# Performance work log

Measured on AMD Instinct MI355X. Metric: run time of the kernel, lower is better.

Reference implementation:

```python
import jax, jax.numpy as jnp
import numpy as np
import math

EPS = 1.1920929e-07  # torch F.rms_norm default eps = fp32 machine epsilon


def rms_norm(x):
    # normalize over last dim, no learned weight (matches F.rms_norm(x, (d,)))
    var = jnp.mean(jnp.square(x), axis=-1, keepdims=True)
    return x * jax.lax.rsqrt(var + EPS)


def rotary(x, cos, sin):
    # x: (B, T, H, D); cos/sin: (T, D) -> broadcast over B, H
    d2 = x.shape[-1] // 2
    x1, x2 = x[..., :d2], x[..., d2:]
    rot = jnp.concatenate([-x2, x1], axis=-1)  # rotate_half
    c = cos[None, :, None, :]
    s = sin[None, :, None, :]
    return x * c + rot * s


def setup_inputs() -> dict:
    key = jax.random.key(0)
    ks = jax.random.split(key, 5)
    B, T, C, H = 2, 2048, 1024, 16
    D = C // H
    x = jax.random.normal(ks[0], (B, T, C), dtype=jnp.float32)
    # real RoPE tables (theta=10000), duplicated across the two halves
    inv_freq = 1.0 / (10000.0 ** (np.arange(0, D, 2, dtype=np.float32) / D))
    pos = np.arange(T, dtype=np.float32)
    freqs = np.outer(pos, inv_freq)            # (T, D/2)
    emb = np.concatenate([freqs, freqs], -1)   # (T, D)
    cos = jnp.asarray(np.cos(emb), dtype=jnp.float32)
    sin = jnp.asarray(np.sin(emb), dtype=jnp.float32)
    sc_in = 1.0 / math.sqrt(C)
    W_attn = jax.random.normal(ks[1], (C, 3 * C), dtype=jnp.float32) * sc_in
    b_attn = jax.random.normal(ks[2], (3 * C,), dtype=jnp.float32) * 0.02
    W_proj = jax.random.normal(ks[3], (C, C), dtype=jnp.float32) * sc_in
    b_proj = jax.random.normal(ks[4], (C,), dtype=jnp.float32) * 0.02
    return {"x": x, "cos": cos, "sin": sin, "W_attn": W_attn, "b_attn": b_attn,
            "W_proj": W_proj, "b_proj": b_proj}


def reference(x, cos, sin, W_attn, b_attn, W_proj, b_proj):
    B, T, C = x.shape
    H = 16
    D = C // H
    qkv = x @ W_attn + b_attn                         # (B, T, 3C)
    qkv = qkv.reshape(B, T, 3, H, D)                  # 'b t (a h d) -> ...'
    q, k, v = qkv[:, :, 0], qkv[:, :, 1], qkv[:, :, 2]  # (B, T, H, D)
    q, k = rms_norm(q), rms_norm(k)
    q = rotary(q, cos, sin)
    k = rotary(k, cos, sin)
    # causal SDPA, scale = 1/sqrt(D)
    scale = 1.0 / math.sqrt(D)
    scores = jnp.einsum('bthd,bshd->bhts', q, k) * scale  # (B, H, T, T)
    causal = jnp.tril(jnp.ones((T, T), dtype=bool))
    scores = jnp.where(causal[None, None], scores, jnp.finfo(scores.dtype).min)
    attn = jax.nn.softmax(scores, axis=-1)
    y = jnp.einsum('bhts,bshd->bthd', attn, v)            # (B, T, H, D)
    y = y.reshape(B, T, C)
    return y @ W_proj + b_proj
```

## Files before the change

### kernel.cpp

```cpp
#include <hip/hip_runtime.h>
#include <math.h>

#define EPSV 1.1920929e-07f

typedef __attribute__((ext_vector_type(8))) short short8;
typedef __attribute__((ext_vector_type(4))) float f32x4;

__device__ __forceinline__ float bf2f(unsigned short u) {
    union { unsigned int i; float f; } c; c.i = ((unsigned int)u) << 16; return c.f;
}
__device__ __forceinline__ unsigned short f2bf(float f) {
    union { float f; unsigned int i; } c; c.f = f;
    unsigned int r = c.i + 0x7FFFu + ((c.i >> 16) & 1u);
    return (unsigned short)(r >> 16);
}
__device__ __forceinline__ unsigned int pack_bf16_ru(float a, float b) {
    union { float f; unsigned int i; } ca, cb; ca.f = a; cb.f = b;
    return __builtin_amdgcn_perm(cb.i + 0x8000u, ca.i + 0x8000u, 0x07060302u);
}
__device__ __forceinline__ void async_lds16(const unsigned short* g, unsigned short* l) {
    __builtin_amdgcn_global_load_lds(
        (const __attribute__((address_space(1))) unsigned int*)g,
        (__attribute__((address_space(3))) unsigned int*)l, 16, 0, 0);
}

__global__ __launch_bounds__(256) void cast_bf16(
    const float* __restrict__ src, unsigned short* __restrict__ dst, int n)
{
    const int i = (blockIdx.x * 256 + threadIdx.x) * 4;
    if (i >= n) return;
    const float4 v = *(const float4*)&src[i];
    ushort4 o;
    o.x = f2bf(v.x); o.y = f2bf(v.y); o.z = f2bf(v.z); o.w = f2bf(v.w);
    *(ushort4*)&dst[i] = o;
}

__global__ __launch_bounds__(256) void transpose_cast_both(
    const float* __restrict__ Wa, unsigned short* __restrict__ Wat,
    const float* __restrict__ Wp, unsigned short* __restrict__ Wpt)
{
    __shared__ float tile[32][33];
    int bx = blockIdx.x;
    const float* W; unsigned short* Wt; int N;
    if (bx < 96) { W = Wa; Wt = Wat; N = 3072; }
    else         { W = Wp; Wt = Wpt; N = 1024; bx -= 96; }
    const int n0 = bx * 32, k0 = blockIdx.y * 32;
    const int r = threadIdx.x >> 3, c4 = (threadIdx.x & 7) * 4;
    const float4 v = *(const float4*)&W[(size_t)(k0 + r) * N + n0 + c4];
    tile[r][c4 + 0] = v.x; tile[r][c4 + 1] = v.y;
    tile[r][c4 + 2] = v.z; tile[r][c4 + 3] = v.w;
    __syncthreads();
    ushort4 o;
    o.x = f2bf(tile[c4 + 0][r]); o.y = f2bf(tile[c4 + 1][r]);
    o.z = f2bf(tile[c4 + 2][r]); o.w = f2bf(tile[c4 + 3][r]);
    *(ushort4*)&Wt[(size_t)(n0 + r) * 1024 + k0 + c4] = o;
}

template <bool OUT_BF16>
__global__ __launch_bounds__(256) void gemm_bf16(
    const unsigned short* __restrict__ A,
    const unsigned short* __restrict__ Bt,
    const float* __restrict__ bias,
    void* __restrict__ Cv,
    int M, int N, int K)
{
    __shared__ unsigned short As0[128][32], As1[128][32];
    __shared__ unsigned short Bs0[128][32], Bs1[128][32];
    const int t    = threadIdx.x;
    const int lane = t & 63;
    const int wv   = t >> 6;
    const int wrow = (wv >> 1) * 64;
    const int wcol = (wv & 1) * 64;
    const int m0 = blockIdx.y * 128;
    const int n0 = blockIdx.x * 128;
    const int col  = lane & 15;
    const int quad = lane >> 4;

    const int srow = (wv << 5) + (lane >> 2);
    const int scol = (lane & 3) << 3;
    const unsigned short* a00 = A  + (size_t)(m0 + srow) * K + scol;
    const unsigned short* a10 = a00 + (size_t)16 * K;
    const unsigned short* a01 = a00 + 32;
    const unsigned short* a11 = a10 + 32;
    const unsigned short* b00 = Bt + (size_t)(n0 + srow) * K + scol;
    const unsigned short* b10 = b00 + (size_t)16 * K;
    const unsigned short* b01 = b00 + 32;
    const unsigned short* b11 = b10 + 32;
    unsigned short* al0 = &As0[srow][scol];
    unsigned short* al1 = &As0[srow + 16][scol];
    unsigned short* al2 = &As1[srow][scol];
    unsigned short* al3 = &As1[srow + 16][scol];
    unsigned short* bl0 = &Bs0[srow][scol];
    unsigned short* bl1 = &Bs0[srow + 16][scol];
    unsigned short* bl2 = &Bs1[srow][scol];
    unsigned short* bl3 = &Bs1[srow + 16][scol];

    f32x4 acc[4][4];
    #pragma unroll
    for (int i = 0; i < 4; ++i)
        #pragma unroll
        for (int j = 0; j < 4; ++j)
            acc[i][j] = (f32x4){0.f, 0.f, 0.f, 0.f};

    for (int k0 = 0; k0 < K; k0 += 64) {
        async_lds16(a00, al0);
        async_lds16(a10, al1);
        async_lds16(a01, al2);
        async_lds16(a11, al3);
        async_lds16(b00, bl0);
        async_lds16(b10, bl1);
        async_lds16(b01, bl2);
        async_lds16(b11, bl3);
        a00 += 64; a10 += 64; a01 += 64; a11 += 64;
        b00 += 64; b10 += 64; b01 += 64; b11 += 64;
        __syncthreads();
        short8 af[2][4], bf[2][4];
        #pragma unroll
        for (int mt = 0; mt < 4; ++mt) {
            af[0][mt] = *(const short8*)&As0[wrow + mt * 16 + col][quad << 3];
            af[1][mt] = *(const short8*)&As1[wrow + mt * 16 + col][quad << 3];
        }
        #pragma unroll
        for (int nt = 0; nt < 4; ++nt) {
            bf[0][nt] = *(const short8*)&Bs0[wcol + nt * 16 + col][quad << 3];
            bf[1][nt] = *(const short8*)&Bs1[wcol + nt * 16 + col][quad << 3];
        }
        #pragma unroll
        for (int ks = 0; ks < 2; ++ks)
            #pragma unroll
            for (int mt = 0; mt < 4; ++mt)
                #pragma unroll
                for (int nt = 0; nt < 4; ++nt)
                    acc[mt][nt] = __builtin_amdgcn_mfma_f32_16x16x32_bf16(
                        af[ks][mt], bf[ks][nt], acc[mt][nt], 0, 0, 0);
        __syncthreads();
    }

    const int rowq = quad << 2;
    #pragma unroll
    for (int nt = 0; nt < 4; ++nt) {
        const int n = n0 + wcol + nt * 16 + col;
        const float bv = bias[n];
        #pragma unroll
        for (int mt = 0; mt < 4; ++mt) {
            #pragma unroll
            for (int r = 0; r < 4; ++r) {
                const int m = m0 + wrow + mt * 16 + rowq + r;
                const float v = acc[mt][nt][r] + bv;
                if (OUT_BF16)
                    ((unsigned short*)Cv)[(size_t)m * N + n] = f2bf(v);
                else
                    ((float*)Cv)[(size_t)m * N + n] = v;
            }
        }
    }
}

__global__ __launch_bounds__(256) void gemm_bf16_n64(
    const unsigned short* __restrict__ A,
    const unsigned short* __restrict__ Bt,
    const float* __restrict__ bias,
    float* __restrict__ C,
    int M, int N, int K)
{
    __shared__ unsigned short As0[128][32], As1[128][32];
    __shared__ unsigned short Bs0[64][32], Bs1[64][32];
    const int t    = threadIdx.x;
    const int lane = t & 63;
    const int wv   = t >> 6;
    const int wrow = wv << 5;
    const int m0 = blockIdx.y * 128;
    const int n0 = blockIdx.x * 64;
    const int col  = lane & 15;
    const int quad = lane >> 4;

    const int srow = (wv << 5) + (lane >> 2);
    const int scol = (lane & 3) << 3;
    const unsigned short* a00 = A  + (size_t)(m0 + srow) * K + scol;
    const unsigned short* a10 = a00 + (size_t)16 * K;
    const unsigned short* a01 = a00 + 32;
    const unsigned short* a11 = a10 + 32;
    const int bsrow = (wv << 4) + (lane >> 2);
    const unsigned short* b00 = Bt + (size_t)(n0 + bsrow) * K + scol;
    const unsigned short* b01 = b00 + 32;
    unsigned short* al0 = &As0[srow][scol];
    unsigned short* al1 = &As0[srow + 16][scol];
    unsigned short* al2 = &As1[srow][scol];
    unsigned short* al3 = &As1[srow + 16][scol];
    unsigned short* bl0 = &Bs0[bsrow][scol];
    unsigned short* bl1 = &Bs1[bsrow][scol];

    f32x4 acc[2][4];
    #pragma unroll
    for (int i = 0; i < 2; ++i)
        #pragma unroll
        for (int j = 0; j < 4; ++j)
            acc[i][j] = (f32x4){0.f, 0.f, 0.f, 0.f};

    for (int k0 = 0; k0 < K; k0 += 64) {
        async_lds16(a00, al0);
        async_lds16(a10, al1);
        async_lds16(a01, al2);
        async_lds16(a11, al3);
        async_lds16(b00, bl0);
        async_lds16(b01, bl1);
        a00 += 64; a10 += 64; a01 += 64; a11 += 64;
        b00 += 64; b01 += 64;
        __syncthreads();
        short8 af[2][2], bf[2][4];
        #pragma unroll
        for (int mt = 0; mt < 2; ++mt) {
            af[0][mt] = *(const short8*)&As0[wrow + mt * 16 + col][quad << 3];
            af[1][mt] = *(const short8*)&As1[wrow + mt * 16 + col][quad << 3];
        }
        #pragma unroll
        for (int nt = 0; nt < 4; ++nt) {
            bf[0][nt] = *(const short8*)&Bs0[nt * 16 + col][quad << 3];
            bf[1][nt] = *(const short8*)&Bs1[nt * 16 + col][quad << 3];
        }
        #pragma unroll
        for (int ks = 0; ks < 2; ++ks)
            #pragma unroll
            for (int mt = 0; mt < 2; ++mt)
                #pragma unroll
                for (int nt = 0; nt < 4; ++nt)
                    acc[mt][nt] = __builtin_amdgcn_mfma_f32_16x16x32_bf16(
                        af[ks][mt], bf[ks][nt], acc[mt][nt], 0, 0, 0);
        __syncthreads();
    }

    const int rowq = quad << 2;
    #pragma unroll
    for (int nt = 0; nt < 4; ++nt) {
        const int n = n0 + nt * 16 + col;
        const float bv = bias[n];
        #pragma unroll
        for (int mt = 0; mt < 2; ++mt) {
            #pragma unroll
            for (int r = 0; r < 4; ++r) {
                const int m = m0 + wrow + mt * 16 + rowq + r;
                C[(size_t)m * N + n] = acc[mt][nt][r] + bv;
            }
        }
    }
}

__global__ __launch_bounds__(256) void rmsnorm_rope(
    unsigned short* __restrict__ qkv, const float* __restrict__ cosp,
    const float* __restrict__ sinp, int BT, int T)
{
    const int wid  = (blockIdx.x << 2) + (threadIdx.x >> 6);
    const int lane = threadIdx.x & 63;
    const int hq = wid & 3;
    const int w  = (wid >> 2) & 1;
    const int bt = wid >> 3;
    if (bt >= BT) return;
    const int h  = (hq << 2) + (lane >> 4);
    const int d4 = (lane & 15) << 2;
    const int tpos = bt % T;
    const size_t idx = (size_t)bt * 3072 + (w << 10) + (h << 6) + d4;

    const ushort4 u = *(const ushort4*)&qkv[idx];
    const float x0 = bf2f(u.x), x1 = bf2f(u.y), x2 = bf2f(u.z), x3 = bf2f(u.w);
    float ss = x0 * x0 + x1 * x1 + x2 * x2 + x3 * x3;
    ss += __shfl_xor(ss, 1, 64);
    ss += __shfl_xor(ss, 2, 64);
    ss += __shfl_xor(ss, 4, 64);
    ss += __shfl_xor(ss, 8, 64);
    const float rn = rsqrtf(ss * (1.0f / 64.0f) + EPSV);
    const float xn0 = x0 * rn, xn1 = x1 * rn, xn2 = x2 * rn, xn3 = x3 * rn;
    const float p0 = __shfl_xor(xn0, 8, 64);
    const float p1 = __shfl_xor(xn1, 8, 64);
    const float p2 = __shfl_xor(xn2, 8, 64);
    const float p3 = __shfl_xor(xn3, 8, 64);
    const float sgn = (d4 < 32) ? -1.0f : 1.0f;
    const float4 c = *(const float4*)&cosp[tpos * 64 + d4];
    const float4 s = *(const float4*)&sinp[tpos * 64 + d4];
    const float scale = (w == 0) ? 0.18033688011112042f : 1.0f;
    ushort4 o;
    o.x = f2bf(fmaf(xn0, c.x, sgn * p0 * s.x) * scale);
    o.y = f2bf(fmaf(xn1, c.y, sgn * p1 * s.y) * scale);
    o.z = f2bf(fmaf(xn2, c.z, sgn * p2 * s.z) * scale);
    o.w = f2bf(fmaf(xn3, c.w, sgn * p3 * s.w) * scale);
    *(ushort4*)&qkv[idx] = o;
}

__global__ __launch_bounds__(256) void v_transpose(
    const unsigned short* __restrict__ qkv, unsigned short* __restrict__ vt,
    int T)
{
    __shared__ unsigned short tile[64][72];
    const int bh = blockIdx.x;
    const int b  = bh >> 4, h = bh & 15;
    const int t0 = blockIdx.y << 6;
    const int t  = threadIdx.x;
    const unsigned short* vbase = qkv + (size_t)b * T * 3072 + 2048 + (h << 6);

    #pragma unroll
    for (int i = 0; i < 2; ++i) {
        const int c = t + (i << 8);
        const int r = c >> 3, c8 = (c & 7) << 3;
        const short8 v = *(const short8*)&vbase[(size_t)(t0 + r) * 3072 + c8];
        #pragma unroll
        for (int j = 0; j < 8; ++j)
            tile[c8 + j][r] = (unsigned short)v[j];
    }
    __syncthreads();
    #pragma unroll
    for (int i = 0; i < 2; ++i) {
        const int c = t + (i << 8);
        const int d = c >> 3, c8 = (c & 7) << 3;
        const short8 o = *(const short8*)&tile[d][c8];
        *(short8*)&vt[((size_t)bh * 64 + d) * T + t0 + c8] = o;
    }
}

__global__ __launch_bounds__(256) void flash_attn_mfma(
    const unsigned short* __restrict__ qkv,
    const unsigned short* __restrict__ vt,
    unsigned short* __restrict__ yb,
    int B, int T)
{
    const int bh = blockIdx.x;
    const int b  = bh >> 4, h = bh & 15;
    const int q0 = ((int)gridDim.y - 1 - (int)blockIdx.y) << 6;
    const int t  = threadIdx.x;
    const int lane = t & 63;
    const int w    = t >> 6;
    const int col  = lane & 15;
    const int quad = lane >> 4;

    __shared__ unsigned short Ks [64][72];
    __shared__ unsigned short Vts[64][72];
    __shared__ unsigned short Ps [4][16][72];

    const unsigned short* qb  = qkv + (size_t)b * T * 3072 + (h << 6);
    const unsigned short* kb  = qb + 1024;
    const unsigned short* vtb = vt + (size_t)bh * 64 * T;

    const int qw = q0 + w * 16;
    const int qg = qw + col;

    short8 qf[2];
    {
        const unsigned short* qrow = qb + (size_t)qg * 3072 + (quad << 3);
        qf[0] = *(const short8*)&qrow[0];
        qf[1] = *(const short8*)&qrow[32];
    }

    f32x4 oacc[4];
    #pragma unroll
    for (int i = 0; i < 4; ++i) oacc[i] = (f32x4){0.f, 0.f, 0.f, 0.f};
    float l_i = 0.f;

    const int sr = t >> 3, sc = (t & 7) << 3;
    const unsigned short* kp0 = kb  + (size_t)sr * 3072 + sc;
    const unsigned short* kp1 = kp0 + (size_t)32 * 3072;
    const unsigned short* vp0 = vtb + (size_t)sr * T + sc;
    const unsigned short* vp1 = vp0 + (size_t)32 * T;
    unsigned short* kw0 = &Ks[sr][sc];
    unsigned short* kw1 = &Ks[sr + 32][sc];
    unsigned short* vw0 = &Vts[sr][sc];
    unsigned short* vw1 = &Vts[sr + 32][sc];
    unsigned short* pw  = &Ps[w][col][0];

    short8 rk0 = *(const short8*)kp0;
    short8 rk1 = *(const short8*)kp1;
    short8 rv0 = *(const short8*)vp0;
    short8 rv1 = *(const short8*)vp1;

    const int last_kt = q0 >> 6;
    for (int kt = 0; kt <= last_kt; ++kt) {
        const int k0 = kt << 6;
        __syncthreads();
        *(short8*)kw0 = rk0;
        *(short8*)kw1 = rk1;
        *(short8*)vw0 = rv0;
        *(short8*)vw1 = rv1;
        __syncthreads();
        if (kt < last_kt) {
            kp0 += 64 * 3072; kp1 += 64 * 3072; vp0 += 64; vp1 += 64;
            rk0 = *(const short8*)kp0;
            rk1 = *(const short8*)kp1;
            rv0 = *(const short8*)vp0;
            rv1 = *(const short8*)vp1;
        }

        f32x4 st[4];
        #pragma unroll
        for (int i = 0; i < 4; ++i) st[i] = (f32x4){0.f, 0.f, 0.f, 0.f};
        #pragma unroll
        for (int ks = 0; ks < 2; ++ks)
            #pragma unroll
            for (int mt = 0; mt < 4; ++mt) {
                const short8 kf = *(const short8*)&Ks[mt * 16 + col][ks * 32 + (quad << 3)];
                st[mt] = __builtin_amdgcn_mfma_f32_16x16x32_bf16(kf, qf[ks], st[mt], 0, 0, 0);
            }

        const bool diag = (k0 + 63 > qw);
        float rs = 0.f;
        #pragma unroll
        for (int mt = 0; mt < 4; ++mt) {
            float x0 = st[mt][0], x1 = st[mt][1], x2 = st[mt][2], x3 = st[mt][3];
            if (diag) {
                const int sbase = k0 + mt * 16 + (quad << 2);
                if (sbase + 0 > qg) x0 = -INFINITY;
                if (sbase + 1 > qg) x1 = -INFINITY;
                if (sbase + 2 > qg) x2 = -INFINITY;
                if (sbase + 3 > qg) x3 = -INFINITY;
            }
            const float p0 = __builtin_amdgcn_exp2f(x0);
            const float p1 = __builtin_amdgcn_exp2f(x1);
            const float p2 = __builtin_amdgcn_exp2f(x2);
            const float p3 = __builtin_amdgcn_exp2f(x3);
            rs += (p0 + p1) + (p2 + p3);
            uint2 pk;
            pk.x = pack_bf16_ru(p0, p1);
            pk.y = pack_bf16_ru(p2, p3);
            *(uint2*)&pw[mt * 16 + (quad << 2)] = pk;
        }
        rs += __shfl_xor(rs, 16, 64);
        rs += __shfl_xor(rs, 32, 64);
        l_i += rs;

        #pragma unroll
        for (int ks = 0; ks < 2; ++ks) {
            const short8 pf = *(const short8*)&pw[ks * 32 + (quad << 3)];
            #pragma unroll
            for (int mt = 0; mt < 4; ++mt) {
                const short8 vf = *(const short8*)&Vts[mt * 16 + col][ks * 32 + (quad << 3)];
                oacc[mt] = __builtin_amdgcn_mfma_f32_16x16x32_bf16(vf, pf, oacc[mt], 0, 0, 0);
            }
        }
    }

    const float inv = 1.0f / l_i;
    unsigned short* yrow = yb + (size_t)(b * T + qg) * 1024 + (h << 6);
    #pragma unroll
    for (int mt = 0; mt < 4; ++mt) {
        ushort4 yv;
        yv.x = f2bf(oacc[mt][0] * inv);
        yv.y = f2bf(oacc[mt][1] * inv);
        yv.z = f2bf(oacc[mt][2] * inv);
        yv.w = f2bf(oacc[mt][3] * inv);
        *(ushort4*)&yrow[mt * 16 + (quad << 2)] = yv;
    }
}

extern "C" void kernel_launch(void* const* d_in, const int* in_sizes, int n_in,
                              void* d_out, int out_size, void* d_ws, size_t ws_size,
                              hipStream_t stream)
{
    const float* x      = (const float*)d_in[0];
    const float* cosp   = (const float*)d_in[1];
    const float* sinp   = (const float*)d_in[2];
    const float* W_attn = (const float*)d_in[3];
    const float* b_attn = (const float*)d_in[4];
    const float* W_proj = (const float*)d_in[5];
    const float* b_proj = (const float*)d_in[6];
    float* out = (float*)d_out;

    const int C = 1024, H = 16;
    const int T  = in_sizes[1] / 64;
    const int BT = in_sizes[0] / C;
    const int B  = BT / T;

    unsigned short* qkvb = (unsigned short*)d_ws;
    unsigned short* xb   = qkvb + (size_t)BT * 3072;
    unsigned short* Wab  = xb   + (size_t)BT * 1024;
    unsigned short* Wpb  = Wab  + (size_t)3072 * 1024;
    unsigned short* yb   = Wpb  + (size_t)1024 * 1024;
    unsigned short* vtb  = xb;

    cast_bf16<<<dim3(BT * C / 1024), dim3(256), 0, stream>>>(x, xb, BT * C);
    transpose_cast_both<<<dim3(128, 32), dim3(256), 0, stream>>>(
        W_attn, Wab, W_proj, Wpb);

    gemm_bf16<true><<<dim3(3 * C / 128, BT / 128), dim3(256), 0, stream>>>(
        xb, Wab, b_attn, qkvb, BT, 3 * C, C);

    rmsnorm_rope<<<dim3(BT * 2), dim3(256), 0, stream>>>(
        qkvb, cosp, sinp, BT, T);

    v_transpose<<<dim3(B * H, T / 64), dim3(256), 0, stream>>>(qkvb, vtb, T);

    flash_attn_mfma<<<dim3(B * H, T / 64), dim3(256), 0, stream>>>(
        qkvb, vtb, yb, B, T);

    gemm_bf16_n64<<<dim3(C / 64, BT / 128), dim3(256), 0, stream>>>(
        yb, Wpb, b_proj, out, BT, C, C);
}
```

Measured before the change: 194.1 us.

## Double query rows per flash-attention block to reuse K/V tiles

Each block of the flash attention kernel now handles 128 query rows instead of 64, with each wave owning two 16-row query chunks. Every K and V tile loaded into LDS then feeds twice as many MFMA operations, and the grid is halved. Waves whose rows are all masked for the final key tile skip its compute. The cost is higher register pressure (two sets of accumulators), an occupancy hint of 3 in launch_bounds, fewer blocks to spread across CUs, and some load imbalance on the diagonal tiles.

```diff
diff --git a/kernel.cpp b/kernel.cpp
--- a/kernel.cpp
+++ b/kernel.cpp
@@ -315,7 +315,7 @@
     }
 }
 
-__global__ __launch_bounds__(256) void flash_attn_mfma(
+__global__ __launch_bounds__(256, 3) void flash_attn_mfma(
     const unsigned short* __restrict__ qkv,
     const unsigned short* __restrict__ vt,
     unsigned short* __restrict__ yb,
@@ -323,7 +323,7 @@
 {
     const int bh = blockIdx.x;
     const int b  = bh >> 4, h = bh & 15;
-    const int q0 = ((int)gridDim.y - 1 - (int)blockIdx.y) << 6;
+    const int q0 = ((int)gridDim.y - 1 - (int)blockIdx.y) << 7;
     const int t  = threadIdx.x;
     const int lane = t & 63;
     const int w    = t >> 6;
@@ -332,26 +332,32 @@
 
     __shared__ unsigned short Ks [64][72];
     __shared__ unsigned short Vts[64][72];
-    __shared__ unsigned short Ps [4][16][72];
+    __shared__ unsigned short Ps [4][32][72];
 
     const unsigned short* qb  = qkv + (size_t)b * T * 3072 + (h << 6);
     const unsigned short* kb  = qb + 1024;
     const unsigned short* vtb = vt + (size_t)bh * 64 * T;
 
-    const int qw = q0 + w * 16;
-    const int qg = qw + col;
-
-    short8 qf[2];
+    const int qw  = q0 + (w << 5);
+    const int qg0 = qw + col;
+    const int qg1 = qw + 16 + col;
+
+    short8 qf[2][2];
     {
-        const unsigned short* qrow = qb + (size_t)qg * 3072 + (quad << 3);
-        qf[0] = *(const short8*)&qrow[0];
-        qf[1] = *(const short8*)&qrow[32];
-    }
-
-    f32x4 oacc[4];
-    #pragma unroll
-    for (int i = 0; i < 4; ++i) oacc[i] = (f32x4){0.f, 0.f, 0.f, 0.f};
-    float l_i = 0.f;
+        const unsigned short* qrow0 = qb + (size_t)qg0 * 3072 + (quad << 3);
+        qf[0][0] = *(const short8*)&qrow0[0];
+        qf[0][1] = *(const short8*)&qrow0[32];
+        const unsigned short* qrow1 = qb + (size_t)qg1 * 3072 + (quad << 3);
+        qf[1][0] = *(const short8*)&qrow1[0];
+        qf[1][1] = *(const short8*)&qrow1[32];
+    }
+
+    f32x4 oacc[2][4];
+    #pragma unroll
+    for (int qc = 0; qc < 2; ++qc)
+        #pragma unroll
+        for (int i = 0; i < 4; ++i) oacc[qc][i] = (f32x4){0.f, 0.f, 0.f, 0.f};
+    float l_i[2] = {0.f, 0.f};
 
     const int sr = t >> 3, sc = (t & 7) << 3;
     const unsigned short* kp0 = kb  + (size_t)sr * 3072 + sc;
@@ -362,14 +368,13 @@
     unsigned short* kw1 = &Ks[sr + 32][sc];
     unsigned short* vw0 = &Vts[sr][sc];
     unsigned short* vw1 = &Vts[sr + 32][sc];
-    unsigned short* pw  = &Ps[w][col][0];
 
     short8 rk0 = *(const short8*)kp0;
     short8 rk1 = *(const short8*)kp1;
     short8 rv0 = *(const short8*)vp0;
     short8 rv1 = *(const short8*)vp1;
 
-    const int last_kt = q0 >> 6;
+    const int last_kt = (q0 + 127) >> 6;
     for (int kt = 0; kt <= last_kt; ++kt) {
         const int k0 = kt << 6;
         __syncthreads();
@@ -386,64 +391,84 @@
             rv1 = *(const short8*)vp1;
         }
 
-        f32x4 st[4];
-        #pragma unroll
-        for (int i = 0; i < 4; ++i) st[i] = (f32x4){0.f, 0.f, 0.f, 0.f};
+        if (k0 > qw + 31) continue;
+
+        f32x4 st[2][4];
+        #pragma unroll
+        for (int qc = 0; qc < 2; ++qc)
+            #pragma unroll
+            for (int i = 0; i < 4; ++i) st[qc][i] = (f32x4){0.f, 0.f, 0.f, 0.f};
         #pragma unroll
         for (int ks = 0; ks < 2; ++ks)
             #pragma unroll
             for (int mt = 0; mt < 4; ++mt) {
                 const short8 kf = *(const short8*)&Ks[mt * 16 + col][ks * 32 + (quad << 3)];
-                st[mt] = __builtin_amdgcn_mfma_f32_16x16x32_bf16(kf, qf[ks], st[mt], 0, 0, 0);
+                st[0][mt] = __builtin_amdgcn_mfma_f32_16x16x32_bf16(kf, qf[0][ks], st[0][mt], 0, 0, 0);
+                st[1][mt] = __builtin_amdgcn_mfma_f32_16x16x32_bf16(kf, qf[1][ks], st[1][mt], 0, 0, 0);
             }
 
-        const bool diag = (k0 + 63 > qw);
-        float rs = 0.f;
-        #pragma unroll
-        for (int mt = 0; mt < 4; ++mt) {
-            float x0 = st[mt][0], x1 = st[mt][1], x2 = st[mt][2], x3 = st[mt][3];
-            if (diag) {
-                const int sbase = k0 + mt * 16 + (quad << 2);
-                if (sbase + 0 > qg) x0 = -INFINITY;
-                if (sbase + 1 > qg) x1 = -INFINITY;
-                if (sbase + 2 > qg) x2 = -INFINITY;
-                if (sbase + 3 > qg) x3 = -INFINITY;
+        #pragma unroll
+        for (int qc = 0; qc < 2; ++qc) {
+            const int qg = qw + (qc << 4) + col;
+            const bool diag = (k0 + 63 > qw + (qc << 4));
+            unsigned short* pw = &Ps[w][(qc << 4) + col][0];
+            float rs = 0.f;
+            #pragma unroll
+            for (int mt = 0; mt < 4; ++mt) {
+                float x0 = st[qc][mt][0], x1 = st[qc][mt][1];
+                float x2 = st[qc][mt][2], x3 = st[qc][mt][3];
+                if (diag) {
+                    const int sbase = k0 + mt * 16 + (quad << 2);
+                    if (sbase + 0 > qg) x0 = -INFINITY;
+                    if (sbase + 1 > qg) x1 = -INFINITY;
+                    if (sbase + 2 > qg) x2 = -INFINITY;
+                    if (sbase + 3 > qg) x3 = -INFINITY;
+                }
+                const float p0 = __builtin_amdgcn_exp2f(x0);
+                const float p1 = __builtin_amdgcn_exp2f(x1);
+                const float p2 = __builtin_amdgcn_exp2f(x2);
+                const float p3 = __builtin_amdgcn_exp2f(x3);
+                rs += (p0 + p1) + (p2 + p3);
+                uint2 pk;
+                pk.x = pack_bf16_ru(p0, p1);
+                pk.y = pack_bf16_ru(p2, p3);
+                *(uint2*)&pw[mt * 16 + (quad << 2)] = pk;
             }
-            const float p0 = __builtin_amdgcn_exp2f(x0);
-            const float p1 = __builtin_amdgcn_exp2f(x1);
-            const float p2 = __builtin_amdgcn_exp2f(x2);
-            const float p3 = __builtin_amdgcn_exp2f(x3);
-            rs += (p0 + p1) + (p2 + p3);
-            uint2 pk;
-            pk.x = pack_bf16_ru(p0, p1);
-            pk.y = pack_bf16_ru(p2, p3);
-            *(uint2*)&pw[mt * 16 + (quad << 2)] = pk;
-        }
-        rs += __shfl_xor(rs, 16, 64);
-        rs += __shfl_xor(rs, 32, 64);
-        l_i += rs;
+            rs += __shfl_xor(rs, 16, 64);
+            rs += __shfl_xor(rs, 32, 64);
+            l_i[qc] += rs;
+        }
 
         #pragma unroll
         for (int ks = 0; ks < 2; ++ks) {
-            const short8 pf = *(const short8*)&pw[ks * 32 + (quad << 3)];
+            const short8 pf0 = *(const short8*)&Ps[w][col][ks * 32 + (quad << 3)];
+            const short8 pf1 = *(const short8*)&Ps[w][16 + col][ks * 32 + (quad << 3)];
             #pragma unroll
             for (int mt = 0; mt < 4; ++mt) {
                 const short8 vf = *(const short8*)&Vts[mt * 16 + col][ks * 32 + (quad << 3)];
-                oacc[mt] = __builtin_amdgcn_mfma_f32_16x16x32_bf16(vf, pf, oacc[mt], 0, 0, 0);
+                oacc[0][mt] = __builtin_amdgcn_mfma_f32_16x16x32_bf16(vf, pf0, oacc[0][mt], 0, 0, 0);
+                oacc[1][mt] = __builtin_amdgcn_mfma_f32_16x16x32_bf16(vf, pf1, oacc[1][mt], 0, 0, 0);
             }
         }
     }
 
-    const float inv = 1.0f / l_i;
-    unsigned short* yrow = yb + (size_t)(b * T + qg) * 1024 + (h << 6);
+    const float inv0 = 1.0f / l_i[0];
+    const float inv1 = 1.0f / l_i[1];
+    unsigned short* yrow0 = yb + (size_t)(b * T + qg0) * 1024 + (h << 6);
+    unsigned short* yrow1 = yb + (size_t)(b * T + qg1) * 1024 + (h << 6);
     #pragma unroll
     for (int mt = 0; mt < 4; ++mt) {
-        ushort4 yv;
-        yv.x = f2bf(oacc[mt][0] * inv);
-        yv.y = f2bf(oacc[mt][1] * inv);
-        yv.z = f2bf(oacc[mt][2] * inv);
-        yv.w = f2bf(oacc[mt][3] * inv);
-        *(ushort4*)&yrow[mt * 16 + (quad << 2)] = yv;
+        ushort4 yv0, yv1;
+        yv0.x = f2bf(oacc[0][mt][0] * inv0);
+        yv0.y = f2bf(oacc[0][mt][1] * inv0);
+        yv0.z = f2bf(oacc[0][mt][2] * inv0);
+        yv0.w = f2bf(oacc[0][mt][3] * inv0);
+        yv1.x = f2bf(oacc[1][mt][0] * inv1);
+        yv1.y = f2bf(oacc[1][mt][1] * inv1);
+        yv1.z = f2bf(oacc[1][mt][2] * inv1);
+        yv1.w = f2bf(oacc[1][mt][3] * inv1);
+        *(ushort4*)&yrow0[mt * 16 + (quad << 2)] = yv0;
+        *(ushort4*)&yrow1[mt * 16 + (quad << 2)] = yv1;
     }
 }
 
@@ -484,7 +509,7 @@
 
     v_transpose<<<dim3(B * H, T / 64), dim3(256), 0, stream>>>(qkvb, vtb, T);
 
-    flash_attn_mfma<<<dim3(B * H, T / 64), dim3(256), 0, stream>>>(
+    flash_attn_mfma<<<dim3(B * H, T / 128), dim3(256), 0, stream>>>(
         qkvb, vtb, yb, B, T);
 
     gemm_bf16_n64<<<dim3(C / 64, BT / 128), dim3(256), 0, stream>>>(
```

After: 202.6 us. 1.04x slower.

## Double-buffer K/V via async LDS loads with 128-row Q tiles per block

Applied to the files above, without the earlier changes.

The causal flash-attention kernel now runs 512 threads per block, so each block covers 128 query rows with eight waves. K and V^T tiles are streamed with direct global-to-LDS async loads into a double buffer, using an XOR swizzle on the column groups, instead of staging through registers. It also raises wave priority around the MFMA sections, skips tiles that lie entirely above the diagonal for a given wave, and interleaves long and short query blocks in launch order. The aim is to overlap K/V loads with compute, cut LDS bank conflicts and balance causal work across blocks, at the cost of more LDS per block and possible occupancy limits.

```diff
diff --git a/kernel.cpp b/kernel.cpp
--- a/kernel.cpp
+++ b/kernel.cpp
@@ -315,7 +315,7 @@
     }
 }
 
-__global__ __launch_bounds__(256) void flash_attn_mfma(
+__global__ __launch_bounds__(512, 4) void flash_attn_mfma(
     const unsigned short* __restrict__ qkv,
     const unsigned short* __restrict__ vt,
     unsigned short* __restrict__ yb,
@@ -323,22 +323,27 @@
 {
     const int bh = blockIdx.x;
     const int b  = bh >> 4, h = bh & 15;
-    const int q0 = ((int)gridDim.y - 1 - (int)blockIdx.y) << 6;
+    const int ny = (int)gridDim.y;
+    const int y  = (int)blockIdx.y;
+    const int hny = (ny + 1) >> 1;
+    const int jq = (y < hny) ? (ny - 1 - y) : (y - hny);
+    const int q0 = jq << 7;
     const int t  = threadIdx.x;
     const int lane = t & 63;
     const int w    = t >> 6;
     const int col  = lane & 15;
     const int quad = lane >> 4;
 
-    __shared__ unsigned short Ks [64][72];
-    __shared__ unsigned short Vts[64][72];
-    __shared__ unsigned short Ps [4][16][72];
+    __shared__ __align__(16) unsigned short smem[25600];
+    unsigned short* Kb = smem;
+    unsigned short* Vb = smem + 8192;
+    unsigned short* Ps = smem + 16384;
 
     const unsigned short* qb  = qkv + (size_t)b * T * 3072 + (h << 6);
     const unsigned short* kb  = qb + 1024;
     const unsigned short* vtb = vt + (size_t)bh * 64 * T;
 
-    const int qw = q0 + w * 16;
+    const int qw = q0 + (w << 4);
     const int qg = qw + col;
 
     short8 qf[2];
@@ -353,85 +358,87 @@
     for (int i = 0; i < 4; ++i) oacc[i] = (f32x4){0.f, 0.f, 0.f, 0.f};
     float l_i = 0.f;
 
-    const int sr = t >> 3, sc = (t & 7) << 3;
-    const unsigned short* kp0 = kb  + (size_t)sr * 3072 + sc;
-    const unsigned short* kp1 = kp0 + (size_t)32 * 3072;
-    const unsigned short* vp0 = vtb + (size_t)sr * T + sc;
-    const unsigned short* vp1 = vp0 + (size_t)32 * T;
-    unsigned short* kw0 = &Ks[sr][sc];
-    unsigned short* kw1 = &Ks[sr + 32][sc];
-    unsigned short* vw0 = &Vts[sr][sc];
-    unsigned short* vw1 = &Vts[sr + 32][sc];
-    unsigned short* pw  = &Ps[w][col][0];
-
-    short8 rk0 = *(const short8*)kp0;
-    short8 rk1 = *(const short8*)kp1;
-    short8 rv0 = *(const short8*)vp0;
-    short8 rv1 = *(const short8*)vp1;
-
-    const int last_kt = q0 >> 6;
+    const int sr = t >> 3;
+    const int sg = (((t & 7) ^ (sr & 7)) << 3);
+    const unsigned short* kp = kb  + (size_t)sr * 3072 + sg;
+    const unsigned short* vp = vtb + (size_t)sr * T + sg;
+
+    async_lds16(kp, Kb + (t << 3));
+    async_lds16(vp, Vb + (t << 3));
+    kp += (size_t)64 * 3072; vp += 64;
+
+    const int cs0 = ((quad ^ (col & 7)) << 3);
+    const int cs1 = (((4 + quad) ^ (col & 7)) << 3);
+
+    const int last_kt = (q0 + 127) >> 6;
+    int cur = 0;
     for (int kt = 0; kt <= last_kt; ++kt) {
         const int k0 = kt << 6;
         __syncthreads();
-        *(short8*)kw0 = rk0;
-        *(short8*)kw1 = rk1;
-        *(short8*)vw0 = rv0;
-        *(short8*)vw1 = rv1;
-        __syncthreads();
         if (kt < last_kt) {
-            kp0 += 64 * 3072; kp1 += 64 * 3072; vp0 += 64; vp1 += 64;
-            rk0 = *(const short8*)kp0;
-            rk1 = *(const short8*)kp1;
-            rv0 = *(const short8*)vp0;
-            rv1 = *(const short8*)vp1;
-        }
-
-        f32x4 st[4];
-        #pragma unroll
-        for (int i = 0; i < 4; ++i) st[i] = (f32x4){0.f, 0.f, 0.f, 0.f};
-        #pragma unroll
-        for (int ks = 0; ks < 2; ++ks)
+            async_lds16(kp, Kb + ((cur ^ 1) << 12) + (t << 3));
+            async_lds16(vp, Vb + ((cur ^ 1) << 12) + (t << 3));
+            kp += (size_t)64 * 3072; vp += 64;
+        }
+
+        if (k0 <= qw + 15) {
+            const unsigned short* Kc = Kb + (cur << 12);
+            const unsigned short* Vc = Vb + (cur << 12);
+
+            f32x4 st[4];
+            #pragma unroll
+            for (int i = 0; i < 4; ++i) st[i] = (f32x4){0.f, 0.f, 0.f, 0.f};
+            __builtin_amdgcn_s_setprio(1);
+            #pragma unroll
+            for (int ks = 0; ks < 2; ++ks)
+                #pragma unroll
+                for (int mt = 0; mt < 4; ++mt) {
+                    const short8 kf = *(const short8*)&Kc[(mt * 16 + col) * 64 + (ks ? cs1 : cs0)];
+                    st[mt] = __builtin_amdgcn_mfma_f32_16x16x32_bf16(kf, qf[ks], st[mt], 0, 0, 0);
+                }
+            __builtin_amdgcn_s_setprio(0);
+
+            const bool diag = (k0 + 63 > qw);
+            unsigned short* pw = Ps + ((w << 4) + col) * 72;
+            float rs = 0.f;
             #pragma unroll
             for (int mt = 0; mt < 4; ++mt) {
-                const short8 kf = *(const short8*)&Ks[mt * 16 + col][ks * 32 + (quad << 3)];
-                st[mt] = __builtin_amdgcn_mfma_f32_16x16x32_bf16(kf, qf[ks], st[mt], 0, 0, 0);
+                float x0 = st[mt][0], x1 = st[mt][1];
+                float x2 = st[mt][2], x3 = st[mt][3];
+                if (diag) {
+                    const int sbase = k0 + mt * 16 + (quad << 2);
+                    if (sbase + 0 > qg) x0 = -INFINITY;
+                    if (sbase + 1 > qg) x1 = -INFINITY;
+                    if (sbase + 2 > qg) x2 = -INFINITY;
+                    if (sbase + 3 > qg) x3 = -INFINITY;
+                }
+                const float p0 = __builtin_amdgcn_exp2f(x0);
+                const float p1 = __builtin_amdgcn_exp2f(x1);
+                const float p2 = __builtin_amdgcn_exp2f(x2);
+                const float p3 = __builtin_amdgcn_exp2f(x3);
+                rs += (p0 + p1) + (p2 + p3);
+                uint2 pk;
+                pk.x = pack_bf16_ru(p0, p1);
+                pk.y = pack_bf16_ru(p2, p3);
+                *(uint2*)&pw[mt * 16 + (quad << 2)] = pk;
             }
-
-        const bool diag = (k0 + 63 > qw);
-        float rs = 0.f;
-        #pragma unroll
-        for (int mt = 0; mt < 4; ++mt) {
-            float x0 = st[mt][0], x1 = st[mt][1], x2 = st[mt][2], x3 = st[mt][3];
-            if (diag) {
-                const int sbase = k0 + mt * 16 + (quad << 2);
-                if (sbase + 0 > qg) x0 = -INFINITY;
-                if (sbase + 1 > qg) x1 = -INFINITY;
-                if (sbase + 2 > qg) x2 = -INFINITY;
-                if (sbase + 3 > qg) x3 = -INFINITY;
+            rs += __shfl_xor(rs, 16, 64);
+            rs += __shfl_xor(rs, 32, 64);
+            l_i += rs;
+
+            __builtin_amdgcn_s_setprio(1);
+            #pragma unroll
+            for (int ks = 0; ks < 2; ++ks) {
+                const short8 pf = *(const short8*)&Ps[((w << 4) + col) * 72 + ks * 32 + (quad << 3)];
+                #pragma unroll
+                for (int mt = 0; mt < 4; ++mt) {
+                    const short8 vf = *(const short8*)&Vc[(mt * 16 + col) * 64 + (ks ? cs1 : cs0)];
+                    oacc[mt] = __builtin_amdgcn_mfma_f32_16x16x32_bf16(vf, pf, oacc[mt], 0, 0, 0);
+                }
             }
-            const float p0 = __builtin_amdgcn_exp2f(x0);
-            const float p1 = __builtin_amdgcn_exp2f(x1);
-            const float p2 = __builtin_amdgcn_exp2f(x2);
-            const float p3 = __builtin_amdgcn_exp2f(x3);
-            rs += (p0 + p1) + (p2 + p3);
-            uint2 pk;
-            pk.x = pack_bf16_ru(p0, p1);
-            pk.y = pack_bf16_ru(p2, p3);
-            *(uint2*)&pw[mt * 16 + (quad << 2)] = pk;
-        }
-        rs += __shfl_xor(rs, 16, 64);
-        rs += __shfl_xor(rs, 32, 64);
-        l_i += rs;
-
-        #pragma unroll
-        for (int ks = 0; ks < 2; ++ks) {
-            const short8 pf = *(const short8*)&pw[ks * 32 + (quad << 3)];
-            #pragma unroll
-            for (int mt = 0; mt < 4; ++mt) {
-                const short8 vf = *(const short8*)&Vts[mt * 16 + col][ks * 32 + (quad << 3)];
-                oacc[mt] = __builtin_amdgcn_mfma_f32_16x16x32_bf16(vf, pf, oacc[mt], 0, 0, 0);
-            }
-        }
+            __builtin_amdgcn_s_setprio(0);
+        }
+        cur ^= 1;
     }
 
     const float inv = 1.0f / l_i;
@@ -484,7 +491,7 @@
 
     v_transpose<<<dim3(B * H, T / 64), dim3(256), 0, stream>>>(qkvb, vtb, T);
 
-    flash_attn_mfma<<<dim3(B * H, T / 64), dim3(256), 0, stream>>>(
+    flash_attn_mfma<<<dim3(B * H, T / 128), dim3(512), 0, stream>>>(
         qkvb, vtb, yb, B, T);
 
     gemm_bf16_n64<<<dim3(C / 64, BT / 128), dim3(256), 0, stream>>>(
```

Result: faster. 189.6 us (-2.3%).
